# Optimization experiments

Hardware: AMD Instinct MI355X
Metric: run time of the kernel (lower is better)

Reference implementation:

```python
import jax, jax.numpy as jnp
import numpy as np
from jax import lax

B, C_IN, H = 64, 3, 64
K_FEAT, KSIZE, STRIDE = 24, 8, 8
G_IN, G_HID, F_HID, OUT = 52, 256, 256, 1


def setup_inputs() -> dict:
    key = jax.random.key(0)
    ks = jax.random.split(key, 8)
    s = lambda fan_in: 1.0 / np.sqrt(fan_in)
    return {
        "image": jax.random.normal(ks[0], (B, C_IN, H, H), jnp.float32),
        "conv_w": jax.random.normal(ks[1], (K_FEAT, C_IN, KSIZE, KSIZE), jnp.float32) * s(C_IN * KSIZE * KSIZE),
        "conv_b": jnp.zeros((K_FEAT,), jnp.float32),
        "g_w1": jax.random.normal(ks[2], (G_IN, G_HID), jnp.float32) * s(G_IN),
        "g_b1": jnp.zeros((G_HID,), jnp.float32),
        "g_w2": jax.random.normal(ks[3], (G_HID, G_HID), jnp.float32) * s(G_HID),
        "g_b2": jnp.zeros((G_HID,), jnp.float32),
        "f_w1": jax.random.normal(ks[4], (G_HID, F_HID), jnp.float32) * s(G_HID),
        "f_b1": jnp.zeros((F_HID,), jnp.float32),
        "f_w2": jax.random.normal(ks[5], (F_HID, OUT), jnp.float32) * s(F_HID),
        "f_b2": jnp.zeros((OUT,), jnp.float32),
    }


def reference(image, conv_w, conv_b, g_w1, g_b1, g_w2, g_b2, f_w1, f_b1, f_w2, f_b2):
    # feature_extractor: conv k8/s8 + ReLU -> (B, k, d, d)
    x = lax.conv_general_dilated(image, conv_w, (STRIDE, STRIDE), "VALID",
                                 dimension_numbers=("NCHW", "OIHW", "NCHW"))
    x = jax.nn.relu(x + conv_b[None, :, None, None])
    b, k, d, _ = x.shape
    # coordinate channels: x varies along columns, y along rows (linspace(-1,1,d))
    coord = jnp.linspace(-1.0, 1.0, d, dtype=x.dtype)
    cx = jnp.broadcast_to(coord[None, None, None, :], (b, 1, d, d))
    cy = jnp.broadcast_to(coord[None, None, :, None], (b, 1, d, d))
    x = jnp.concatenate([x, cx, cy], axis=1)          # (B, k+2, d, d)
    k2 = k + 2
    x = x.reshape(b, k2, d * d).transpose(0, 2, 1)     # (B, d^2, k+2)
    # all-pairs: pair (i, j) -> concat(x[:, j], x[:, i])  (matches repeat/cat in torch)
    left = jnp.broadcast_to(x[:, None, :, :], (b, d * d, d * d, k2))
    right = jnp.broadcast_to(x[:, :, None, :], (b, d * d, d * d, k2))
    pairs = jnp.concatenate([left, right], axis=-1)    # (B, d^2, d^2, 2(k+2))
    # g: shared MLP over pairs
    h = jax.nn.relu(pairs @ g_w1 + g_b1)
    h = jax.nn.relu(h @ g_w2 + g_b2)                   # (B, d^2, d^2, 256)
    pooled = jnp.sum(h, axis=(1, 2))                   # sum over d^4 pairs -> (B, 256)
    # f: head MLP
    h = jax.nn.relu(pooled @ f_w1 + f_b1)
    return h @ f_w2 + f_b2                             # (B, 1)
```

## Files before the change

### kernel.cpp

```cpp
#include <hip/hip_runtime.h>
#include <hip/hip_bf16.h>
#include <stdint.h>


typedef float f32x4 __attribute__((ext_vector_type(4)));
typedef float f32x2 __attribute__((ext_vector_type(2)));
typedef short short8 __attribute__((ext_vector_type(8)));
typedef int   int4v  __attribute__((ext_vector_type(4)));

__device__ __forceinline__ uint32_t cvt_pk_bf16(float lo, float hi) {
    uint32_t r;
    asm("v_cvt_pk_bf16_f32 %0, %1, %2" : "=v"(r) : "v"(lo), "v"(hi));
    return r;
}
__device__ __forceinline__ f32x2 relu2(f32x2 a) {
    f32x2 z = (f32x2){0.f, 0.f};
    return __builtin_elementwise_max(a, z);
}

__global__ void k12_front(const float* __restrict__ img, const float* __restrict__ cw,
                          const float* __restrict__ cb, const float* __restrict__ w1,
                          const float* __restrict__ b1, const float* __restrict__ w2,
                          float* __restrict__ u, float* __restrict__ v,
                          short* __restrict__ w2f) {
    int g = blockIdx.x;
    int t = threadIdx.x;
    if (g >= 256) {
        int fi = (g - 256) * 4 + (t >> 6);
        int l = t & 63;
        int ks = fi >> 4, ni2 = fi & 15;
        int n  = ni2 * 16 + (l & 15);
        int k0 = ks * 32 + (l >> 4) * 8;
        float f[8];
        #pragma unroll
        for (int e = 0; e < 8; ++e) f[e] = w2[(k0 + e) * 256 + n];
        union { short8 s; uint32_t w[4]; } A;
        A.w[0] = cvt_pk_bf16(f[0], f[1]);
        A.w[1] = cvt_pk_bf16(f[2], f[3]);
        A.w[2] = cvt_pk_bf16(f[4], f[5]);
        A.w[3] = cvt_pk_bf16(f[6], f[7]);
        *(short8*)(w2f + (fi * 64 + l) * 8) = A.s;
        return;
    }
    __shared__ float xs[16][26];
    int b = g >> 2, q = g & 3, p0 = q * 16;

    for (int idx = t; idx < 416; idx += 256) {
        int pl = idx / 26;
        int ch = idx - pl * 26;
        int pos = p0 + pl;
        int r = pos >> 3, c = pos & 7;
        float val;
        if (ch < 24) {
            float s = cb[ch];
            #pragma unroll
            for (int ci = 0; ci < 3; ++ci)
                #pragma unroll
                for (int kr = 0; kr < 8; ++kr) {
                    const float* ip = img + ((b * 3 + ci) * 64 + r * 8 + kr) * 64 + c * 8;
                    const float* wp = cw + ((ch * 3 + ci) * 8 + kr) * 8;
                    #pragma unroll
                    for (int kc = 0; kc < 8; ++kc) s += ip[kc] * wp[kc];
                }
            val = fmaxf(s, 0.f);
        } else if (ch == 24) {
            val = -1.f + (2.f / 7.f) * (float)c;
        } else {
            val = -1.f + (2.f / 7.f) * (float)r;
        }
        xs[pl][ch] = val;
    }
    __syncthreads();

    int c = t;
    float bc = b1[c];
    float su[16], sv[16];
    #pragma unroll
    for (int r = 0; r < 16; ++r) { su[r] = bc; sv[r] = 0.f; }
    #pragma unroll 2
    for (int k = 0; k < 26; ++k) {
        float wu = w1[k * 256 + c];
        float wv2 = w1[(26 + k) * 256 + c];
        #pragma unroll
        for (int r = 0; r < 16; ++r) {
            float xv = xs[r][k];
            su[r] += xv * wu;
            sv[r] += xv * wv2;
        }
    }
    #pragma unroll
    for (int r = 0; r < 16; ++r) {
        int bj = b * 64 + p0 + r;
        u[bj * 256 + c] = su[r];
        v[bj * 256 + c] = sv[r];
    }
}

#define STAGE(Q, BUF)                                                  \
{                                                                      \
    f32x4 va = *(const f32x4*)&vs[Q][col8 * 8];                        \
    f32x4 vb = *(const f32x4*)&vs[Q][col8 * 8 + 4];                    \
    _Pragma("unroll")                                                  \
    for (int rr = 0; rr < 4; ++rr) {                                   \
        f32x2 a0 = relu2((f32x2){u0[rr].x, u0[rr].y} + (f32x2){va.x, va.y}); \
        f32x2 a1 = relu2((f32x2){u0[rr].z, u0[rr].w} + (f32x2){va.z, va.w}); \
        f32x2 a2 = relu2((f32x2){u1[rr].x, u1[rr].y} + (f32x2){vb.x, vb.y}); \
        f32x2 a3 = relu2((f32x2){u1[rr].z, u1[rr].w} + (f32x2){vb.z, vb.w}); \
        int4v d;                                                       \
        d.x = (int)cvt_pk_bf16(a0.x, a0.y);                            \
        d.y = (int)cvt_pk_bf16(a1.x, a1.y);                            \
        d.z = (int)cvt_pk_bf16(a2.x, a2.y);                            \
        d.w = (int)cvt_pk_bf16(a3.x, a3.y);                            \
        *(int4v*)((char*)(BUF) + wb[rr]) = d;                          \
    }                                                                  \
}

#define MFMA_KS(KS)                                                   \
    { const char* hx = ((KS) & 1) ? hO : hE;                          \
      short8 a0 = *(const short8*)(hx + ((KS) >> 1) * 128);           \
      short8 a1 = *(const short8*)(hx + 8192 + ((KS) >> 1) * 128);    \
      acc[0][0] = __builtin_amdgcn_mfma_f32_16x16x32_bf16(a0, Bf[KS][0], acc[0][0], 0, 0, 0); \
      acc[1][0] = __builtin_amdgcn_mfma_f32_16x16x32_bf16(a1, Bf[KS][0], acc[1][0], 0, 0, 0); \
      acc[0][1] = __builtin_amdgcn_mfma_f32_16x16x32_bf16(a0, Bf[KS][1], acc[0][1], 0, 0, 0); \
      acc[1][1] = __builtin_amdgcn_mfma_f32_16x16x32_bf16(a1, Bf[KS][1], acc[1][1], 0, 0, 0); \
      acc[0][2] = __builtin_amdgcn_mfma_f32_16x16x32_bf16(a0, Bf[KS][2], acc[0][2], 0, 0, 0); \
      acc[1][2] = __builtin_amdgcn_mfma_f32_16x16x32_bf16(a1, Bf[KS][2], acc[1][2], 0, 0, 0); \
      acc[0][3] = __builtin_amdgcn_mfma_f32_16x16x32_bf16(a0, Bf[KS][3], acc[0][3], 0, 0, 0); \
      acc[1][3] = __builtin_amdgcn_mfma_f32_16x16x32_bf16(a1, Bf[KS][3], acc[1][3], 0, 0, 0); }

__global__ __launch_bounds__(512, 2) void k3_pairs(
        const float* __restrict__ u, const float* __restrict__ v,
        const short* __restrict__ w2f, const float* __restrict__ b2,
        float* __restrict__ part) {
    __shared__ short h1s[2][64 * 256];
    __shared__ float vs[16][256];
    int t = threadIdx.x;
    int lane = t & 63, wv = t >> 6;
    int lr = lane & 15, lg = lane >> 4;
    int blk = blockIdx.x;
    int b = blk & 63, i0 = (blk >> 6) * 16;
    int r0 = (wv & 1) * 32;
    int c0 = (wv >> 1) * 64;

    {
        int q = t >> 5, c8 = (t & 31) * 8;
        const float* vr = v + (b * 64 + i0 + q) * 256 + c8;
        *(float4*)&vs[q][c8]     = *(const float4*)vr;
        *(float4*)&vs[q][c8 + 4] = *(const float4*)(vr + 4);
    }

    short8 Bf[8][4];
    #pragma unroll
    for (int ks = 0; ks < 8; ++ks)
        #pragma unroll
        for (int cg = 0; cg < 4; ++cg)
            Bf[ks][cg] = *(const short8*)(w2f + ((ks * 16 + (wv >> 1) * 4 + cg) * 64 + lane) * 8);

    f32x2 bias2[4];
    #pragma unroll
    for (int cg = 0; cg < 4; ++cg) {
        float bv = b2[c0 + cg * 16 + lr];
        bias2[cg] = (f32x2){bv, bv};
    }

    int col8 = t & 31, rq = t >> 5;
    const float* up = u + (b * 64 + rq * 4) * 256 + col8 * 8;
    f32x4 u0[4], u1[4];
    int wb[4];
    #pragma unroll
    for (int rr = 0; rr < 4; ++rr) {
        u0[rr] = *(const f32x4*)(up + rr * 256);
        u1[rr] = *(const f32x4*)(up + rr * 256 + 4);
        int row = rq * 4 + rr;
        wb[rr] = row * 512 + ((col8 * 16) ^ ((row & 7) << 4));
    }

    int XB = (lg * 16) ^ ((lr & 7) << 4);
    int rE = (r0 + lr) * 512 + XB;
    int rO = (r0 + lr) * 512 + (XB ^ 64);

    __syncthreads();
    STAGE(0, h1s[0])
    __syncthreads();

    f32x2 csum2[4];
    #pragma unroll
    for (int cg = 0; cg < 4; ++cg) csum2[cg] = (f32x2){0.f, 0.f};

    #pragma unroll 1
    for (int q = 0; q < 16; ++q) {
        if (q < 15) STAGE(q + 1, h1s[(q + 1) & 1])

        const char* hE = (const char*)h1s[q & 1] + rE;
        const char* hO = (const char*)h1s[q & 1] + rO;

        f32x4 acc[2][4];
        #pragma unroll
        for (int mi = 0; mi < 2; ++mi)
            #pragma unroll
            for (int cg = 0; cg < 4; ++cg) acc[mi][cg] = (f32x4){0.f, 0.f, 0.f, 0.f};

        __builtin_amdgcn_s_setprio(1);
        MFMA_KS(0) MFMA_KS(1) MFMA_KS(2) MFMA_KS(3)
        MFMA_KS(4) MFMA_KS(5) MFMA_KS(6) MFMA_KS(7)
        __builtin_amdgcn_s_setprio(0);

        #pragma unroll
        for (int cg = 0; cg < 4; ++cg) {
            #pragma unroll
            for (int mi = 0; mi < 2; ++mi) {
                f32x2 lo = relu2((f32x2){acc[mi][cg].x, acc[mi][cg].y} + bias2[cg]);
                f32x2 hi = relu2((f32x2){acc[mi][cg].z, acc[mi][cg].w} + bias2[cg]);
                csum2[cg] = csum2[cg] + lo + hi;
            }
        }
        __syncthreads();
    }

    #pragma unroll
    for (int cg = 0; cg < 4; ++cg) {
        float s = csum2[cg].x + csum2[cg].y;
        s += __shfl_xor(s, 16);
        s += __shfl_xor(s, 32);
        if (lane < 16) part[(blk * 8 + wv) * 64 + cg * 16 + lr] = s;
    }
}

__global__ void k5_head(const float* __restrict__ part, const float* __restrict__ fw1,
                        const float* __restrict__ fb1, const float* __restrict__ fw2,
                        const float* __restrict__ fb2, float* __restrict__ out) {
    __shared__ float P[256];
    __shared__ float wsum[4];
    int b = blockIdx.x, t = threadIdx.x;
    int wpair = (t >> 6) * 2, cl = t & 63;
    float s0 = 0.f;
    #pragma unroll
    for (int tile = 0; tile < 4; ++tile) {
        const float* p = part + (((b + 64 * tile) * 8) + wpair) * 64 + cl;
        s0 += p[0] + p[64];
    }
    P[t] = s0;
    __syncthreads();
    float a0 = 0.f, a1 = 0.f, a2 = 0.f, a3 = 0.f;
    for (int k = 0; k < 64; ++k) {
        a0 += P[k]       * fw1[k * 256 + t];
        a1 += P[k + 64]  * fw1[(k + 64) * 256 + t];
        a2 += P[k + 128] * fw1[(k + 128) * 256 + t];
        a3 += P[k + 192] * fw1[(k + 192) * 256 + t];
    }
    float h = fmaxf(fb1[t] + a0 + a1 + a2 + a3, 0.f);
    float p = h * fw2[t];
    #pragma unroll
    for (int off = 32; off >= 1; off >>= 1) p += __shfl_xor(p, off);
    if ((t & 63) == 0) wsum[t >> 6] = p;
    __syncthreads();
    if (t == 0) out[b] = wsum[0] + wsum[1] + wsum[2] + wsum[3] + fb2[0];
}

extern "C" void kernel_launch(void* const* d_in, const int* in_sizes, int n_in,
                              void* d_out, int out_size, void* d_ws, size_t ws_size,
                              hipStream_t stream) {
    const float* image  = (const float*)d_in[0];
    const float* conv_w = (const float*)d_in[1];
    const float* conv_b = (const float*)d_in[2];
    const float* g_w1   = (const float*)d_in[3];
    const float* g_b1   = (const float*)d_in[4];
    const float* g_w2   = (const float*)d_in[5];
    const float* g_b2   = (const float*)d_in[6];
    const float* f_w1   = (const float*)d_in[7];
    const float* f_b1   = (const float*)d_in[8];
    const float* f_w2   = (const float*)d_in[9];
    const float* f_b2   = (const float*)d_in[10];
    float* out = (float*)d_out;

    char* ws = (char*)d_ws;
    float* u    = (float*)(ws + 0);
    float* v    = (float*)(ws + 4194304);
    short* w2f  = (short*)(ws + 8388608);
    float* part = (float*)(ws + 8519680);

    k12_front<<<288, 256, 0, stream>>>(image, conv_w, conv_b, g_w1, g_b1, g_w2,
                                       u, v, w2f);
    k3_pairs<<<256, 512, 0, stream>>>(u, v, w2f, g_b2, part);
    k5_head<<<64, 256, 0, stream>>>(part, f_w1, f_b1, f_w2, f_b2, out);
}
```

Before: 61.62 us.

## Interleave next-tile staging with MFMA chunks and split v smem layout

```diff
diff --git a/kernel.cpp b/kernel.cpp
--- a/kernel.cpp
+++ b/kernel.cpp
@@ -96,44 +96,39 @@
     }
 }
 
-#define STAGE(Q, BUF)                                                  \
-{                                                                      \
-    f32x4 va = *(const f32x4*)&vs[Q][col8 * 8];                        \
-    f32x4 vb = *(const f32x4*)&vs[Q][col8 * 8 + 4];                    \
-    _Pragma("unroll")                                                  \
-    for (int rr = 0; rr < 4; ++rr) {                                   \
-        f32x2 a0 = relu2((f32x2){u0[rr].x, u0[rr].y} + (f32x2){va.x, va.y}); \
-        f32x2 a1 = relu2((f32x2){u0[rr].z, u0[rr].w} + (f32x2){va.z, va.w}); \
-        f32x2 a2 = relu2((f32x2){u1[rr].x, u1[rr].y} + (f32x2){vb.x, vb.y}); \
-        f32x2 a3 = relu2((f32x2){u1[rr].z, u1[rr].w} + (f32x2){vb.z, vb.w}); \
-        int4v d;                                                       \
-        d.x = (int)cvt_pk_bf16(a0.x, a0.y);                            \
-        d.y = (int)cvt_pk_bf16(a1.x, a1.y);                            \
-        d.z = (int)cvt_pk_bf16(a2.x, a2.y);                            \
-        d.w = (int)cvt_pk_bf16(a3.x, a3.y);                            \
-        *(int4v*)((char*)(BUF) + wb[rr]) = d;                          \
-    }                                                                  \
-}
-
-#define MFMA_KS(KS)                                                   \
+#define READ_A(KS)                                                    \
     { const char* hx = ((KS) & 1) ? hO : hE;                          \
-      short8 a0 = *(const short8*)(hx + ((KS) >> 1) * 128);           \
-      short8 a1 = *(const short8*)(hx + 8192 + ((KS) >> 1) * 128);    \
-      acc[0][0] = __builtin_amdgcn_mfma_f32_16x16x32_bf16(a0, Bf[KS][0], acc[0][0], 0, 0, 0); \
-      acc[1][0] = __builtin_amdgcn_mfma_f32_16x16x32_bf16(a1, Bf[KS][0], acc[1][0], 0, 0, 0); \
-      acc[0][1] = __builtin_amdgcn_mfma_f32_16x16x32_bf16(a0, Bf[KS][1], acc[0][1], 0, 0, 0); \
-      acc[1][1] = __builtin_amdgcn_mfma_f32_16x16x32_bf16(a1, Bf[KS][1], acc[1][1], 0, 0, 0); \
-      acc[0][2] = __builtin_amdgcn_mfma_f32_16x16x32_bf16(a0, Bf[KS][2], acc[0][2], 0, 0, 0); \
-      acc[1][2] = __builtin_amdgcn_mfma_f32_16x16x32_bf16(a1, Bf[KS][2], acc[1][2], 0, 0, 0); \
-      acc[0][3] = __builtin_amdgcn_mfma_f32_16x16x32_bf16(a0, Bf[KS][3], acc[0][3], 0, 0, 0); \
-      acc[1][3] = __builtin_amdgcn_mfma_f32_16x16x32_bf16(a1, Bf[KS][3], acc[1][3], 0, 0, 0); }
+      Aa[(KS) & 1] = *(const short8*)(hx + ((KS) >> 1) * 128);        \
+      Ab[(KS) & 1] = *(const short8*)(hx + 8192 + ((KS) >> 1) * 128); }
+
+#define MFMA_B(KS)                                                    \
+    acc[0][0] = __builtin_amdgcn_mfma_f32_16x16x32_bf16(Aa[(KS)&1], Bf[KS][0], acc[0][0], 0, 0, 0); \
+    acc[1][0] = __builtin_amdgcn_mfma_f32_16x16x32_bf16(Ab[(KS)&1], Bf[KS][0], acc[1][0], 0, 0, 0); \
+    acc[0][1] = __builtin_amdgcn_mfma_f32_16x16x32_bf16(Aa[(KS)&1], Bf[KS][1], acc[0][1], 0, 0, 0); \
+    acc[1][1] = __builtin_amdgcn_mfma_f32_16x16x32_bf16(Ab[(KS)&1], Bf[KS][1], acc[1][1], 0, 0, 0); \
+    acc[0][2] = __builtin_amdgcn_mfma_f32_16x16x32_bf16(Aa[(KS)&1], Bf[KS][2], acc[0][2], 0, 0, 0); \
+    acc[1][2] = __builtin_amdgcn_mfma_f32_16x16x32_bf16(Ab[(KS)&1], Bf[KS][2], acc[1][2], 0, 0, 0); \
+    acc[0][3] = __builtin_amdgcn_mfma_f32_16x16x32_bf16(Aa[(KS)&1], Bf[KS][3], acc[0][3], 0, 0, 0); \
+    acc[1][3] = __builtin_amdgcn_mfma_f32_16x16x32_bf16(Ab[(KS)&1], Bf[KS][3], acc[1][3], 0, 0, 0);
+
+#define PASS(RR)                                                       \
+    { f32x2 a0 = relu2((f32x2){u0[RR].x, u0[RR].y} + (f32x2){va.x, va.y}); \
+      f32x2 a1 = relu2((f32x2){u0[RR].z, u0[RR].w} + (f32x2){va.z, va.w}); \
+      f32x2 a2 = relu2((f32x2){u1[RR].x, u1[RR].y} + (f32x2){vb.x, vb.y}); \
+      f32x2 a3 = relu2((f32x2){u1[RR].z, u1[RR].w} + (f32x2){vb.z, vb.w}); \
+      int4v d;                                                         \
+      d.x = (int)cvt_pk_bf16(a0.x, a0.y);                              \
+      d.y = (int)cvt_pk_bf16(a1.x, a1.y);                              \
+      d.z = (int)cvt_pk_bf16(a2.x, a2.y);                              \
+      d.w = (int)cvt_pk_bf16(a3.x, a3.y);                              \
+      *(int4v*)(wbuf + wb[RR]) = d; }
 
 __global__ __launch_bounds__(512, 2) void k3_pairs(
         const float* __restrict__ u, const float* __restrict__ v,
         const short* __restrict__ w2f, const float* __restrict__ b2,
         float* __restrict__ part) {
     __shared__ short h1s[2][64 * 256];
-    __shared__ float vs[16][256];
+    __shared__ float vs[16][2][128];
     int t = threadIdx.x;
     int lane = t & 63, wv = t >> 6;
     int lr = lane & 15, lg = lane >> 4;
@@ -145,8 +140,8 @@
     {
         int q = t >> 5, c8 = (t & 31) * 8;
         const float* vr = v + (b * 64 + i0 + q) * 256 + c8;
-        *(float4*)&vs[q][c8]     = *(const float4*)vr;
-        *(float4*)&vs[q][c8 + 4] = *(const float4*)(vr + 4);
+        *(float4*)&vs[q][0][(t & 31) * 4] = *(const float4*)vr;
+        *(float4*)&vs[q][1][(t & 31) * 4] = *(const float4*)(vr + 4);
     }
 
     short8 Bf[8][4];
@@ -180,7 +175,13 @@
     int rO = (r0 + lr) * 512 + (XB ^ 64);
 
     __syncthreads();
-    STAGE(0, h1s[0])
+
+    {
+        f32x4 va = *(const f32x4*)&vs[0][0][col8 * 4];
+        f32x4 vb = *(const f32x4*)&vs[0][1][col8 * 4];
+        char* wbuf = (char*)h1s[0];
+        PASS(0) PASS(1) PASS(2) PASS(3)
+    }
     __syncthreads();
 
     f32x2 csum2[4];
@@ -189,10 +190,13 @@
 
     #pragma unroll 1
     for (int q = 0; q < 16; ++q) {
-        if (q < 15) STAGE(q + 1, h1s[(q + 1) & 1])
-
         const char* hE = (const char*)h1s[q & 1] + rE;
         const char* hO = (const char*)h1s[q & 1] + rO;
+        char* wbuf = (char*)h1s[(q + 1) & 1];
+        bool pre = (q < 15);
+        int qn = (q + 1) & 15;
+        f32x4 va = *(const f32x4*)&vs[qn][0][col8 * 4];
+        f32x4 vb = *(const f32x4*)&vs[qn][1][col8 * 4];
 
         f32x4 acc[2][4];
         #pragma unroll
@@ -200,9 +204,27 @@
             #pragma unroll
             for (int cg = 0; cg < 4; ++cg) acc[mi][cg] = (f32x4){0.f, 0.f, 0.f, 0.f};
 
+        short8 Aa[2], Ab[2];
+
+        READ_A(0) READ_A(1)
+        if (pre) PASS(0)
         __builtin_amdgcn_s_setprio(1);
-        MFMA_KS(0) MFMA_KS(1) MFMA_KS(2) MFMA_KS(3)
-        MFMA_KS(4) MFMA_KS(5) MFMA_KS(6) MFMA_KS(7)
+        MFMA_B(0) MFMA_B(1)
+        __builtin_amdgcn_s_setprio(0);
+        READ_A(2) READ_A(3)
+        if (pre) PASS(1)
+        __builtin_amdgcn_s_setprio(1);
+        MFMA_B(2) MFMA_B(3)
+        __builtin_amdgcn_s_setprio(0);
+        READ_A(4) READ_A(5)
+        if (pre) PASS(2)
+        __builtin_amdgcn_s_setprio(1);
+        MFMA_B(4) MFMA_B(5)
+        __builtin_amdgcn_s_setprio(0);
+        READ_A(6) READ_A(7)
+        if (pre) PASS(3)
+        __builtin_amdgcn_s_setprio(1);
+        MFMA_B(6) MFMA_B(7)
         __builtin_amdgcn_s_setprio(0);
 
         #pragma unroll
```

Result: no change. 61.03 us (-0.9%).

## Split pairs kernel into producer and consumer warps with LDS flag pipeline

Applied to the files above, without the earlier changes.

```diff
diff --git a/kernel.cpp b/kernel.cpp
--- a/kernel.cpp
+++ b/kernel.cpp
@@ -8,6 +8,8 @@
 typedef short short8 __attribute__((ext_vector_type(8)));
 typedef int   int4v  __attribute__((ext_vector_type(4)));
 
+#define NB 4
+
 __device__ __forceinline__ uint32_t cvt_pk_bf16(float lo, float hi) {
     uint32_t r;
     asm("v_cvt_pk_bf16_f32 %0, %1, %2" : "=v"(r) : "v"(lo), "v"(hi));
@@ -16,6 +18,16 @@
 __device__ __forceinline__ f32x2 relu2(f32x2 a) {
     f32x2 z = (f32x2){0.f, 0.f};
     return __builtin_elementwise_max(a, z);
+}
+__device__ __forceinline__ void spin_eq(int* p, int val) {
+    while (__hip_atomic_load(p, __ATOMIC_ACQUIRE, __HIP_MEMORY_SCOPE_WORKGROUP) != val)
+        __builtin_amdgcn_s_sleep(1);
+    __builtin_amdgcn_sched_barrier(0);
+}
+__device__ __forceinline__ void flag_release_add(int* p, int lane) {
+    asm volatile("s_waitcnt lgkmcnt(0)" ::: "memory");
+    if (lane == 0)
+        __hip_atomic_fetch_add(p, 1, __ATOMIC_RELEASE, __HIP_MEMORY_SCOPE_WORKGROUP);
 }
 
 __global__ void k12_front(const float* __restrict__ img, const float* __restrict__ cw,
@@ -96,133 +108,158 @@
     }
 }
 
-#define STAGE(Q, BUF)                                                  \
-{                                                                      \
-    f32x4 va = *(const f32x4*)&vs[Q][col8 * 8];                        \
-    f32x4 vb = *(const f32x4*)&vs[Q][col8 * 8 + 4];                    \
-    _Pragma("unroll")                                                  \
-    for (int rr = 0; rr < 4; ++rr) {                                   \
-        f32x2 a0 = relu2((f32x2){u0[rr].x, u0[rr].y} + (f32x2){va.x, va.y}); \
-        f32x2 a1 = relu2((f32x2){u0[rr].z, u0[rr].w} + (f32x2){va.z, va.w}); \
-        f32x2 a2 = relu2((f32x2){u1[rr].x, u1[rr].y} + (f32x2){vb.x, vb.y}); \
-        f32x2 a3 = relu2((f32x2){u1[rr].z, u1[rr].w} + (f32x2){vb.z, vb.w}); \
-        int4v d;                                                       \
-        d.x = (int)cvt_pk_bf16(a0.x, a0.y);                            \
-        d.y = (int)cvt_pk_bf16(a1.x, a1.y);                            \
-        d.z = (int)cvt_pk_bf16(a2.x, a2.y);                            \
-        d.w = (int)cvt_pk_bf16(a3.x, a3.y);                            \
-        *(int4v*)((char*)(BUF) + wb[rr]) = d;                          \
-    }                                                                  \
-}
-
-#define MFMA_KS(KS)                                                   \
-    { const char* hx = ((KS) & 1) ? hO : hE;                          \
-      short8 a0 = *(const short8*)(hx + ((KS) >> 1) * 128);           \
-      short8 a1 = *(const short8*)(hx + 8192 + ((KS) >> 1) * 128);    \
-      acc[0][0] = __builtin_amdgcn_mfma_f32_16x16x32_bf16(a0, Bf[KS][0], acc[0][0], 0, 0, 0); \
-      acc[1][0] = __builtin_amdgcn_mfma_f32_16x16x32_bf16(a1, Bf[KS][0], acc[1][0], 0, 0, 0); \
-      acc[0][1] = __builtin_amdgcn_mfma_f32_16x16x32_bf16(a0, Bf[KS][1], acc[0][1], 0, 0, 0); \
-      acc[1][1] = __builtin_amdgcn_mfma_f32_16x16x32_bf16(a1, Bf[KS][1], acc[1][1], 0, 0, 0); \
-      acc[0][2] = __builtin_amdgcn_mfma_f32_16x16x32_bf16(a0, Bf[KS][2], acc[0][2], 0, 0, 0); \
-      acc[1][2] = __builtin_amdgcn_mfma_f32_16x16x32_bf16(a1, Bf[KS][2], acc[1][2], 0, 0, 0); \
-      acc[0][3] = __builtin_amdgcn_mfma_f32_16x16x32_bf16(a0, Bf[KS][3], acc[0][3], 0, 0, 0); \
-      acc[1][3] = __builtin_amdgcn_mfma_f32_16x16x32_bf16(a1, Bf[KS][3], acc[1][3], 0, 0, 0); }
+#define C_READ(A, KS)                                                  \
+    { const char* hx = ((KS) & 1) ? hO : hE;                           \
+      A[0] = *(const short8*)(hx + ((KS) >> 1) * 128);                 \
+      A[1] = *(const short8*)(hx + 8192  + ((KS) >> 1) * 128);         \
+      A[2] = *(const short8*)(hx + 16384 + ((KS) >> 1) * 128);         \
+      A[3] = *(const short8*)(hx + 24576 + ((KS) >> 1) * 128); }
+
+#define C_MFMA(A, KS)                                                  \
+    { acc[0][0] = __builtin_amdgcn_mfma_f32_16x16x32_bf16(A[0], Bf[KS][0], acc[0][0], 0,0,0); \
+      acc[1][0] = __builtin_amdgcn_mfma_f32_16x16x32_bf16(A[1], Bf[KS][0], acc[1][0], 0,0,0); \
+      acc[2][0] = __builtin_amdgcn_mfma_f32_16x16x32_bf16(A[2], Bf[KS][0], acc[2][0], 0,0,0); \
+      acc[3][0] = __builtin_amdgcn_mfma_f32_16x16x32_bf16(A[3], Bf[KS][0], acc[3][0], 0,0,0); \
+      acc[0][1] = __builtin_amdgcn_mfma_f32_16x16x32_bf16(A[0], Bf[KS][1], acc[0][1], 0,0,0); \
+      acc[1][1] = __builtin_amdgcn_mfma_f32_16x16x32_bf16(A[1], Bf[KS][1], acc[1][1], 0,0,0); \
+      acc[2][1] = __builtin_amdgcn_mfma_f32_16x16x32_bf16(A[2], Bf[KS][1], acc[2][1], 0,0,0); \
+      acc[3][1] = __builtin_amdgcn_mfma_f32_16x16x32_bf16(A[3], Bf[KS][1], acc[3][1], 0,0,0); \
+      acc[0][2] = __builtin_amdgcn_mfma_f32_16x16x32_bf16(A[0], Bf[KS][2], acc[0][2], 0,0,0); \
+      acc[1][2] = __builtin_amdgcn_mfma_f32_16x16x32_bf16(A[1], Bf[KS][2], acc[1][2], 0,0,0); \
+      acc[2][2] = __builtin_amdgcn_mfma_f32_16x16x32_bf16(A[2], Bf[KS][2], acc[2][2], 0,0,0); \
+      acc[3][2] = __builtin_amdgcn_mfma_f32_16x16x32_bf16(A[3], Bf[KS][2], acc[3][2], 0,0,0); \
+      acc[0][3] = __builtin_amdgcn_mfma_f32_16x16x32_bf16(A[0], Bf[KS][3], acc[0][3], 0,0,0); \
+      acc[1][3] = __builtin_amdgcn_mfma_f32_16x16x32_bf16(A[1], Bf[KS][3], acc[1][3], 0,0,0); \
+      acc[2][3] = __builtin_amdgcn_mfma_f32_16x16x32_bf16(A[2], Bf[KS][3], acc[2][3], 0,0,0); \
+      acc[3][3] = __builtin_amdgcn_mfma_f32_16x16x32_bf16(A[3], Bf[KS][3], acc[3][3], 0,0,0); }
 
 __global__ __launch_bounds__(512, 2) void k3_pairs(
         const float* __restrict__ u, const float* __restrict__ v,
         const short* __restrict__ w2f, const float* __restrict__ b2,
         float* __restrict__ part) {
-    __shared__ short h1s[2][64 * 256];
-    __shared__ float vs[16][256];
+    __shared__ short h1s[NB][64 * 256];
+    __shared__ float vs[16][2][128];
+    __shared__ int prod_cnt[16];
+    __shared__ int cons_cnt[16];
     int t = threadIdx.x;
     int lane = t & 63, wv = t >> 6;
-    int lr = lane & 15, lg = lane >> 4;
     int blk = blockIdx.x;
     int b = blk & 63, i0 = (blk >> 6) * 16;
-    int r0 = (wv & 1) * 32;
-    int c0 = (wv >> 1) * 64;
+
+    if (t < 16) { prod_cnt[t] = 0; cons_cnt[t] = 0; }
 
     {
         int q = t >> 5, c8 = (t & 31) * 8;
         const float* vr = v + (b * 64 + i0 + q) * 256 + c8;
-        *(float4*)&vs[q][c8]     = *(const float4*)vr;
-        *(float4*)&vs[q][c8 + 4] = *(const float4*)(vr + 4);
-    }
-
-    short8 Bf[8][4];
-    #pragma unroll
-    for (int ks = 0; ks < 8; ++ks)
-        #pragma unroll
-        for (int cg = 0; cg < 4; ++cg)
-            Bf[ks][cg] = *(const short8*)(w2f + ((ks * 16 + (wv >> 1) * 4 + cg) * 64 + lane) * 8);
-
-    f32x2 bias2[4];
-    #pragma unroll
-    for (int cg = 0; cg < 4; ++cg) {
-        float bv = b2[c0 + cg * 16 + lr];
-        bias2[cg] = (f32x2){bv, bv};
-    }
-
-    int col8 = t & 31, rq = t >> 5;
-    const float* up = u + (b * 64 + rq * 4) * 256 + col8 * 8;
-    f32x4 u0[4], u1[4];
-    int wb[4];
-    #pragma unroll
-    for (int rr = 0; rr < 4; ++rr) {
-        u0[rr] = *(const f32x4*)(up + rr * 256);
-        u1[rr] = *(const f32x4*)(up + rr * 256 + 4);
-        int row = rq * 4 + rr;
-        wb[rr] = row * 512 + ((col8 * 16) ^ ((row & 7) << 4));
-    }
-
-    int XB = (lg * 16) ^ ((lr & 7) << 4);
-    int rE = (r0 + lr) * 512 + XB;
-    int rO = (r0 + lr) * 512 + (XB ^ 64);
-
+        *(float4*)&vs[q][0][(t & 31) * 4] = *(const float4*)vr;
+        *(float4*)&vs[q][1][(t & 31) * 4] = *(const float4*)(vr + 4);
+    }
     __syncthreads();
-    STAGE(0, h1s[0])
-    __syncthreads();
-
-    f32x2 csum2[4];
-    #pragma unroll
-    for (int cg = 0; cg < 4; ++cg) csum2[cg] = (f32x2){0.f, 0.f};
-
-    #pragma unroll 1
-    for (int q = 0; q < 16; ++q) {
-        if (q < 15) STAGE(q + 1, h1s[(q + 1) & 1])
-
-        const char* hE = (const char*)h1s[q & 1] + rE;
-        const char* hO = (const char*)h1s[q & 1] + rO;
-
-        f32x4 acc[2][4];
-        #pragma unroll
-        for (int mi = 0; mi < 2; ++mi)
-            #pragma unroll
-            for (int cg = 0; cg < 4; ++cg) acc[mi][cg] = (f32x4){0.f, 0.f, 0.f, 0.f};
+
+    if (wv < 4) {
+        int col8 = t & 31, rq = t >> 5;
+        const float* up = u + (b * 64 + rq * 8) * 256 + col8 * 8;
+        f32x4 u0[8], u1[8];
+        #pragma unroll
+        for (int rr = 0; rr < 8; ++rr) {
+            u0[rr] = *(const f32x4*)(up + rr * 256);
+            u1[rr] = *(const f32x4*)(up + rr * 256 + 4);
+        }
+        int wbase = rq * 8 * 512;
+        int c16 = col8 * 16;
+
+        #pragma unroll 1
+        for (int q = 0; q < 16; ++q) {
+            if (q >= NB) spin_eq(&cons_cnt[q - NB], 4);
+            char* wbuf = (char*)h1s[q & (NB - 1)] + wbase;
+            f32x4 va = *(const f32x4*)&vs[q][0][col8 * 4];
+            f32x4 vb = *(const f32x4*)&vs[q][1][col8 * 4];
+            #pragma unroll
+            for (int rr = 0; rr < 8; ++rr) {
+                f32x2 a0 = relu2((f32x2){u0[rr].x, u0[rr].y} + (f32x2){va.x, va.y});
+                f32x2 a1 = relu2((f32x2){u0[rr].z, u0[rr].w} + (f32x2){va.z, va.w});
+                f32x2 a2 = relu2((f32x2){u1[rr].x, u1[rr].y} + (f32x2){vb.x, vb.y});
+                f32x2 a3 = relu2((f32x2){u1[rr].z, u1[rr].w} + (f32x2){vb.z, vb.w});
+                int4v d;
+                d.x = (int)cvt_pk_bf16(a0.x, a0.y);
+                d.y = (int)cvt_pk_bf16(a1.x, a1.y);
+                d.z = (int)cvt_pk_bf16(a2.x, a2.y);
+                d.w = (int)cvt_pk_bf16(a3.x, a3.y);
+                *(int4v*)(wbuf + rr * 512 + (c16 ^ (rr << 4))) = d;
+            }
+            flag_release_add(&prod_cnt[q], lane);
+        }
+    } else {
+        int wc = wv - 4;
+        int lr = lane & 15, lg = lane >> 4;
+
+        short8 Bf[8][4];
+        #pragma unroll
+        for (int ks = 0; ks < 8; ++ks)
+            #pragma unroll
+            for (int cg = 0; cg < 4; ++cg)
+                Bf[ks][cg] = *(const short8*)(w2f + ((ks * 16 + wc * 4 + cg) * 64 + lane) * 8);
+
+        f32x2 bias2[4];
+        #pragma unroll
+        for (int cg = 0; cg < 4; ++cg) {
+            float bv = b2[wc * 64 + cg * 16 + lr];
+            bias2[cg] = (f32x2){bv, bv};
+        }
+
+        int XB = (lg * 16) ^ ((lr & 7) << 4);
+        int rE0 = lr * 512 + XB;
+        int rO0 = lr * 512 + (XB ^ 64);
+
+        f32x2 csum2[4];
+        #pragma unroll
+        for (int cg = 0; cg < 4; ++cg) csum2[cg] = (f32x2){0.f, 0.f};
 
         __builtin_amdgcn_s_setprio(1);
-        MFMA_KS(0) MFMA_KS(1) MFMA_KS(2) MFMA_KS(3)
-        MFMA_KS(4) MFMA_KS(5) MFMA_KS(6) MFMA_KS(7)
+        #pragma unroll 1
+        for (int q = 0; q < 16; ++q) {
+            spin_eq(&prod_cnt[q], 4);
+            const char* base = (const char*)h1s[q & (NB - 1)];
+            const char* hE = base + rE0;
+            const char* hO = base + rO0;
+
+            f32x4 acc[4][4];
+            #pragma unroll
+            for (int mi = 0; mi < 4; ++mi)
+                #pragma unroll
+                for (int cg = 0; cg < 4; ++cg) acc[mi][cg] = (f32x4){0.f, 0.f, 0.f, 0.f};
+
+            short8 Aa[4], Ab[4];
+            C_READ(Aa, 0) C_READ(Ab, 1)
+            C_MFMA(Aa, 0) C_READ(Aa, 2)
+            C_MFMA(Ab, 1) C_READ(Ab, 3)
+            C_MFMA(Aa, 2) C_READ(Aa, 4)
+            C_MFMA(Ab, 3) C_READ(Ab, 5)
+            C_MFMA(Aa, 4) C_READ(Aa, 6)
+            C_MFMA(Ab, 5) C_READ(Ab, 7)
+            C_MFMA(Aa, 6)
+            C_MFMA(Ab, 7)
+
+            #pragma unroll
+            for (int cg = 0; cg < 4; ++cg) {
+                #pragma unroll
+                for (int mi = 0; mi < 4; ++mi) {
+                    f32x2 lo = relu2((f32x2){acc[mi][cg].x, acc[mi][cg].y} + bias2[cg]);
+                    f32x2 hi = relu2((f32x2){acc[mi][cg].z, acc[mi][cg].w} + bias2[cg]);
+                    csum2[cg] = csum2[cg] + lo + hi;
+                }
+            }
+            flag_release_add(&cons_cnt[q], lane);
+        }
         __builtin_amdgcn_s_setprio(0);
 
         #pragma unroll
         for (int cg = 0; cg < 4; ++cg) {
-            #pragma unroll
-            for (int mi = 0; mi < 2; ++mi) {
-                f32x2 lo = relu2((f32x2){acc[mi][cg].x, acc[mi][cg].y} + bias2[cg]);
-                f32x2 hi = relu2((f32x2){acc[mi][cg].z, acc[mi][cg].w} + bias2[cg]);
-                csum2[cg] = csum2[cg] + lo + hi;
-            }
-        }
-        __syncthreads();
-    }
-
-    #pragma unroll
-    for (int cg = 0; cg < 4; ++cg) {
-        float s = csum2[cg].x + csum2[cg].y;
-        s += __shfl_xor(s, 16);
-        s += __shfl_xor(s, 32);
-        if (lane < 16) part[(blk * 8 + wv) * 64 + cg * 16 + lr] = s;
+            float s = csum2[cg].x + csum2[cg].y;
+            s += __shfl_xor(s, 16);
+            s += __shfl_xor(s, 32);
+            if (lane < 16) part[(blk * 4 + wc) * 64 + cg * 16 + lr] = s;
+        }
     }
 }
 
@@ -232,13 +269,11 @@
     __shared__ float P[256];
     __shared__ float wsum[4];
     int b = blockIdx.x, t = threadIdx.x;
-    int wpair = (t >> 6) * 2, cl = t & 63;
+    int wc = t >> 6, cl = t & 63;
     float s0 = 0.f;
     #pragma unroll
-    for (int tile = 0; tile < 4; ++tile) {
-        const float* p = part + (((b + 64 * tile) * 8) + wpair) * 64 + cl;
-        s0 += p[0] + p[64];
-    }
+    for (int g = 0; g < 4; ++g)
+        s0 += part[((b + 64 * g) * 4 + wc) * 64 + cl];
     P[t] = s0;
     __syncthreads();
     float a0 = 0.f, a1 = 0.f, a2 = 0.f, a3 = 0.f;
```

New measurement: 60.30 us. -2.1%, faster.

## Build MFMA A-fragments in registers from packed u, dropping LDS h1 staging

Applied to the files above, without the earlier changes.

```diff
diff --git a/kernel.cpp b/kernel.cpp
--- a/kernel.cpp
+++ b/kernel.cpp
@@ -16,6 +16,13 @@
 __device__ __forceinline__ f32x2 relu2(f32x2 a) {
     f32x2 z = (f32x2){0.f, 0.f};
     return __builtin_elementwise_max(a, z);
+}
+__device__ __forceinline__ uint32_t fuse2(uint32_t up, float vlo, float vhi) {
+    f32x2 uu;
+    uu.x = __uint_as_float(up << 16);
+    uu.y = __uint_as_float(up & 0xFFFF0000u);
+    f32x2 r = relu2(uu + (f32x2){vlo, vhi});
+    return cvt_pk_bf16(r.x, r.y);
 }
 
 __global__ void k12_front(const float* __restrict__ img, const float* __restrict__ cw,
@@ -96,51 +103,42 @@
     }
 }
 
-#define STAGE(Q, BUF)                                                  \
-{                                                                      \
-    f32x4 va = *(const f32x4*)&vs[Q][col8 * 8];                        \
-    f32x4 vb = *(const f32x4*)&vs[Q][col8 * 8 + 4];                    \
-    _Pragma("unroll")                                                  \
-    for (int rr = 0; rr < 4; ++rr) {                                   \
-        f32x2 a0 = relu2((f32x2){u0[rr].x, u0[rr].y} + (f32x2){va.x, va.y}); \
-        f32x2 a1 = relu2((f32x2){u0[rr].z, u0[rr].w} + (f32x2){va.z, va.w}); \
-        f32x2 a2 = relu2((f32x2){u1[rr].x, u1[rr].y} + (f32x2){vb.x, vb.y}); \
-        f32x2 a3 = relu2((f32x2){u1[rr].z, u1[rr].w} + (f32x2){vb.z, vb.w}); \
-        int4v d;                                                       \
-        d.x = (int)cvt_pk_bf16(a0.x, a0.y);                            \
-        d.y = (int)cvt_pk_bf16(a1.x, a1.y);                            \
-        d.z = (int)cvt_pk_bf16(a2.x, a2.y);                            \
-        d.w = (int)cvt_pk_bf16(a3.x, a3.y);                            \
-        *(int4v*)((char*)(BUF) + wb[rr]) = d;                          \
-    }                                                                  \
-}
-
-#define MFMA_KS(KS)                                                   \
-    { const char* hx = ((KS) & 1) ? hO : hE;                          \
-      short8 a0 = *(const short8*)(hx + ((KS) >> 1) * 128);           \
-      short8 a1 = *(const short8*)(hx + 8192 + ((KS) >> 1) * 128);    \
-      acc[0][0] = __builtin_amdgcn_mfma_f32_16x16x32_bf16(a0, Bf[KS][0], acc[0][0], 0, 0, 0); \
-      acc[1][0] = __builtin_amdgcn_mfma_f32_16x16x32_bf16(a1, Bf[KS][0], acc[1][0], 0, 0, 0); \
-      acc[0][1] = __builtin_amdgcn_mfma_f32_16x16x32_bf16(a0, Bf[KS][1], acc[0][1], 0, 0, 0); \
-      acc[1][1] = __builtin_amdgcn_mfma_f32_16x16x32_bf16(a1, Bf[KS][1], acc[1][1], 0, 0, 0); \
-      acc[0][2] = __builtin_amdgcn_mfma_f32_16x16x32_bf16(a0, Bf[KS][2], acc[0][2], 0, 0, 0); \
-      acc[1][2] = __builtin_amdgcn_mfma_f32_16x16x32_bf16(a1, Bf[KS][2], acc[1][2], 0, 0, 0); \
-      acc[0][3] = __builtin_amdgcn_mfma_f32_16x16x32_bf16(a0, Bf[KS][3], acc[0][3], 0, 0, 0); \
-      acc[1][3] = __builtin_amdgcn_mfma_f32_16x16x32_bf16(a1, Bf[KS][3], acc[1][3], 0, 0, 0); }
+#define BUILD_FRAG(DST, MI, KS, V0, V1)                                \
+    { int4v d_;                                                        \
+      d_.x = fuse2(upk[MI][KS][0], (V0).x, (V0).y);                    \
+      d_.y = fuse2(upk[MI][KS][1], (V0).z, (V0).w);                    \
+      d_.z = fuse2(upk[MI][KS][2], (V1).x, (V1).y);                    \
+      d_.w = fuse2(upk[MI][KS][3], (V1).z, (V1).w);                    \
+      DST = *(short8*)&d_; }
+
+#define KSTEP(KS)                                                      \
+    { f32x4 V0 = *(const f32x4*)(vq + (KS) * 32 + lg8);                \
+      f32x4 V1 = *(const f32x4*)(vq + (KS) * 32 + lg8 + 4);            \
+      short8 a0, a1;                                                   \
+      BUILD_FRAG(a0, 0, KS, V0, V1)                                    \
+      BUILD_FRAG(a1, 1, KS, V0, V1)                                    \
+      acc[0][0] = __builtin_amdgcn_mfma_f32_16x16x32_bf16(a0, Bf[KS][0], acc[0][0], 0,0,0); \
+      acc[1][0] = __builtin_amdgcn_mfma_f32_16x16x32_bf16(a1, Bf[KS][0], acc[1][0], 0,0,0); \
+      acc[0][1] = __builtin_amdgcn_mfma_f32_16x16x32_bf16(a0, Bf[KS][1], acc[0][1], 0,0,0); \
+      acc[1][1] = __builtin_amdgcn_mfma_f32_16x16x32_bf16(a1, Bf[KS][1], acc[1][1], 0,0,0); \
+      acc[0][2] = __builtin_amdgcn_mfma_f32_16x16x32_bf16(a0, Bf[KS][2], acc[0][2], 0,0,0); \
+      acc[1][2] = __builtin_amdgcn_mfma_f32_16x16x32_bf16(a1, Bf[KS][2], acc[1][2], 0,0,0); \
+      acc[0][3] = __builtin_amdgcn_mfma_f32_16x16x32_bf16(a0, Bf[KS][3], acc[0][3], 0,0,0); \
+      acc[1][3] = __builtin_amdgcn_mfma_f32_16x16x32_bf16(a1, Bf[KS][3], acc[1][3], 0,0,0); }
 
 __global__ __launch_bounds__(512, 2) void k3_pairs(
         const float* __restrict__ u, const float* __restrict__ v,
         const short* __restrict__ w2f, const float* __restrict__ b2,
         float* __restrict__ part) {
-    __shared__ short h1s[2][64 * 256];
     __shared__ float vs[16][256];
     int t = threadIdx.x;
     int lane = t & 63, wv = t >> 6;
     int lr = lane & 15, lg = lane >> 4;
+    int lg8 = lg * 8;
     int blk = blockIdx.x;
     int b = blk & 63, i0 = (blk >> 6) * 16;
-    int r0 = (wv & 1) * 32;
-    int c0 = (wv >> 1) * 64;
+    int wr = wv & 1, wc = wv >> 1;
+    int r0 = wr * 32;
 
     {
         int q = t >> 5, c8 = (t & 31) * 8;
@@ -154,45 +152,39 @@
     for (int ks = 0; ks < 8; ++ks)
         #pragma unroll
         for (int cg = 0; cg < 4; ++cg)
-            Bf[ks][cg] = *(const short8*)(w2f + ((ks * 16 + (wv >> 1) * 4 + cg) * 64 + lane) * 8);
-
-    f32x2 bias2[4];
-    #pragma unroll
-    for (int cg = 0; cg < 4; ++cg) {
-        float bv = b2[c0 + cg * 16 + lr];
-        bias2[cg] = (f32x2){bv, bv};
-    }
-
-    int col8 = t & 31, rq = t >> 5;
-    const float* up = u + (b * 64 + rq * 4) * 256 + col8 * 8;
-    f32x4 u0[4], u1[4];
-    int wb[4];
-    #pragma unroll
-    for (int rr = 0; rr < 4; ++rr) {
-        u0[rr] = *(const f32x4*)(up + rr * 256);
-        u1[rr] = *(const f32x4*)(up + rr * 256 + 4);
-        int row = rq * 4 + rr;
-        wb[rr] = row * 512 + ((col8 * 16) ^ ((row & 7) << 4));
-    }
-
-    int XB = (lg * 16) ^ ((lr & 7) << 4);
-    int rE = (r0 + lr) * 512 + XB;
-    int rO = (r0 + lr) * 512 + (XB ^ 64);
-
-    __syncthreads();
-    STAGE(0, h1s[0])
-    __syncthreads();
-
-    f32x2 csum2[4];
-    #pragma unroll
-    for (int cg = 0; cg < 4; ++cg) csum2[cg] = (f32x2){0.f, 0.f};
+            Bf[ks][cg] = *(const short8*)(w2f + ((ks * 16 + wc * 4 + cg) * 64 + lane) * 8);
+
+    float bias[4];
+    #pragma unroll
+    for (int cg = 0; cg < 4; ++cg) bias[cg] = b2[wc * 64 + cg * 16 + lr];
+
+    uint32_t upk[2][8][4];
+    {
+        const float* ur0 = u + (b * 64 + r0 + lr) * 256 + lg8;
+        const float* ur1 = ur0 + 16 * 256;
+        #pragma unroll
+        for (int ks = 0; ks < 8; ++ks) {
+            f32x4 x0 = *(const f32x4*)(ur0 + ks * 32);
+            f32x4 x1 = *(const f32x4*)(ur0 + ks * 32 + 4);
+            f32x4 y0 = *(const f32x4*)(ur1 + ks * 32);
+            f32x4 y1 = *(const f32x4*)(ur1 + ks * 32 + 4);
+            upk[0][ks][0] = cvt_pk_bf16(x0.x, x0.y);
+            upk[0][ks][1] = cvt_pk_bf16(x0.z, x0.w);
+            upk[0][ks][2] = cvt_pk_bf16(x1.x, x1.y);
+            upk[0][ks][3] = cvt_pk_bf16(x1.z, x1.w);
+            upk[1][ks][0] = cvt_pk_bf16(y0.x, y0.y);
+            upk[1][ks][1] = cvt_pk_bf16(y0.z, y0.w);
+            upk[1][ks][2] = cvt_pk_bf16(y1.x, y1.y);
+            upk[1][ks][3] = cvt_pk_bf16(y1.z, y1.w);
+        }
+    }
+    __syncthreads();
+
+    float csum[4] = {0.f, 0.f, 0.f, 0.f};
 
     #pragma unroll 1
     for (int q = 0; q < 16; ++q) {
-        if (q < 15) STAGE(q + 1, h1s[(q + 1) & 1])
-
-        const char* hE = (const char*)h1s[q & 1] + rE;
-        const char* hO = (const char*)h1s[q & 1] + rO;
+        const float* vq = &vs[q][0];
 
         f32x4 acc[2][4];
         #pragma unroll
@@ -200,26 +192,24 @@
             #pragma unroll
             for (int cg = 0; cg < 4; ++cg) acc[mi][cg] = (f32x4){0.f, 0.f, 0.f, 0.f};
 
-        __builtin_amdgcn_s_setprio(1);
-        MFMA_KS(0) MFMA_KS(1) MFMA_KS(2) MFMA_KS(3)
-        MFMA_KS(4) MFMA_KS(5) MFMA_KS(6) MFMA_KS(7)
-        __builtin_amdgcn_s_setprio(0);
+        KSTEP(0) KSTEP(1) KSTEP(2) KSTEP(3)
+        KSTEP(4) KSTEP(5) KSTEP(6) KSTEP(7)
 
         #pragma unroll
         for (int cg = 0; cg < 4; ++cg) {
+            float s = csum[cg];
             #pragma unroll
-            for (int mi = 0; mi < 2; ++mi) {
-                f32x2 lo = relu2((f32x2){acc[mi][cg].x, acc[mi][cg].y} + bias2[cg]);
-                f32x2 hi = relu2((f32x2){acc[mi][cg].z, acc[mi][cg].w} + bias2[cg]);
-                csum2[cg] = csum2[cg] + lo + hi;
-            }
-        }
-        __syncthreads();
+            for (int mi = 0; mi < 2; ++mi)
+                #pragma unroll
+                for (int r = 0; r < 4; ++r)
+                    s += fmaxf(acc[mi][cg][r] + bias[cg], 0.f);
+            csum[cg] = s;
+        }
     }
 
     #pragma unroll
     for (int cg = 0; cg < 4; ++cg) {
-        float s = csum2[cg].x + csum2[cg].y;
+        float s = csum[cg];
         s += __shfl_xor(s, 16);
         s += __shfl_xor(s, 32);
         if (lane < 16) part[(blk * 8 + wv) * 64 + cg * 16 + lr] = s;
@@ -232,11 +222,11 @@
     __shared__ float P[256];
     __shared__ float wsum[4];
     int b = blockIdx.x, t = threadIdx.x;
-    int wpair = (t >> 6) * 2, cl = t & 63;
+    int wc = t >> 6, cl = t & 63;
     float s0 = 0.f;
     #pragma unroll
-    for (int tile = 0; tile < 4; ++tile) {
-        const float* p = part + (((b + 64 * tile) * 8) + wpair) * 64 + cl;
+    for (int g = 0; g < 4; ++g) {
+        const float* p = part + ((b + 64 * g) * 8 + wc * 2) * 64 + cl;
         s0 += p[0] + p[64];
     }
     P[t] = s0;
```

Result: slower. 117.3 us (+90.3%).
